# Kernel tuning notes

Measured on AMD Instinct MI355X. Metric: run time of the kernel, lower is better.

## Reference

```python
import jax, jax.numpy as jnp
import numpy as np

IN_F, OUT_F, RANK = 4096, 4096, 1024
B, S = 4, 2048


def soft_threshold24(w):
    """Soft-threshold 2:4 sparsification along the last dim.
    For each group of 4, the two smallest-magnitude entries are zeroed and the
    kept entries are shrunk by the threshold (2nd-smallest magnitude)."""
    g = w.reshape(-1, 4)
    m = jnp.abs(g)
    t = jnp.sort(m, axis=-1)[:, 1:2]  # largest pruned magnitude per group
    sp = jnp.sign(g) * jnp.maximum(m - t, 0.0)
    return sp.reshape(w.shape)


def fake_fp8_mm(a, b):
    """FP8-simulated GEMM: fp16 operands, fp32 accumulate/output (matches fake_fp8_mm)."""
    return jnp.matmul(a.astype(jnp.float16), b.astype(jnp.float16),
                      preferred_element_type=jnp.float32)


def setup_inputs() -> dict:
    key = jax.random.key(0)
    k1, k2, k3 = jax.random.split(key, 3)
    x = jax.random.normal(k1, (B, S, IN_F), dtype=jnp.float32)
    std_a = (2.0 / (IN_F + RANK)) ** 0.5   # xavier_normal for (in_features, rank)
    std_b = (2.0 / (OUT_F + RANK)) ** 0.5  # xavier_normal for (out_features, rank)
    weight_A = jax.random.normal(k2, (IN_F, RANK), dtype=jnp.float32) * std_a
    weight_B = jax.random.normal(k3, (OUT_F, RANK), dtype=jnp.float32) * std_b
    bias = jnp.zeros((OUT_F,), dtype=jnp.float32)
    scale_A = jnp.ones((), dtype=jnp.float32)  # sparse_init_scale buffer
    scale_B = jnp.ones((), dtype=jnp.float32)
    return {"x": x, "weight_A": weight_A, "weight_B": weight_B, "bias": bias,
            "scale_A": scale_A, "scale_B": scale_B}


def reference(x, weight_A, weight_B, bias, scale_A, scale_B):
    # sparse low-rank factors
    wa = soft_threshold24(weight_A) * scale_A  # (in, rank)
    wb = soft_threshold24(weight_B) * scale_B  # (out, rank)
    lead = x.shape[:-1]
    xf = x.reshape(-1, x.shape[-1])            # (T, in)
    x_proj = fake_fp8_mm(xf, wa)               # (T, rank) == x @ A_sparse
    out = fake_fp8_mm(x_proj, wb.T) + bias     # (T, out) == x_proj @ B_sparse^T + b
    return out.reshape(*lead, OUT_F)
```

## Files before the change

### kernel.cpp

```cpp
#include <hip/hip_runtime.h>

#define IN_FEAT 4096
#define OUT_FEAT 4096
#define RANK 1024
#define TOK 8192

typedef _Float16 f16x8 __attribute__((ext_vector_type(8)));
typedef _Float16 f16x4 __attribute__((ext_vector_type(4)));
typedef float f32x4 __attribute__((ext_vector_type(4)));

#define GLD_LDS16(g, l)                                                         \
  __builtin_amdgcn_global_load_lds(                                             \
      (__attribute__((address_space(1))) const void*)(g),                       \
      (__attribute__((address_space(3))) void*)(l), 16, 0, 0)


__device__ __forceinline__ void soft24(const float4 g, float s,
                                       float& r0, float& r1, float& r2, float& r3) {
  const float m0 = fabsf(g.x), m1 = fabsf(g.y), m2 = fabsf(g.z), m3 = fabsf(g.w);
  const float lo1 = fminf(m0, m1), hi1 = fmaxf(m0, m1);
  const float lo2 = fminf(m2, m3), hi2 = fmaxf(m2, m3);
  const float t = fminf(fmaxf(lo1, lo2), fminf(hi1, hi2));
  r0 = copysignf(fmaxf(m0 - t, 0.0f), g.x) * s;
  r1 = copysignf(fmaxf(m1 - t, 0.0f), g.y) * s;
  r2 = copysignf(fmaxf(m2 - t, 0.0f), g.z) * s;
  r3 = copysignf(fmaxf(m3 - t, 0.0f), g.w) * s;
}

__global__ __launch_bounds__(256) void sparsify_A_kernel(
    const float* __restrict__ wA, const float* __restrict__ scaleA,
    _Float16* __restrict__ waT) {
  const int idx = blockIdx.x * 256 + threadIdx.x;
  const int i = idx & (IN_FEAT - 1);
  const int jg = idx >> 12;
  const float4 g = *reinterpret_cast<const float4*>(wA + (size_t)i * RANK + jg * 4);
  const float s = scaleA[0];
  float r0, r1, r2, r3;
  soft24(g, s, r0, r1, r2, r3);
  const size_t base = (size_t)(jg * 4) * IN_FEAT + i;
  waT[base] = (_Float16)r0;
  waT[base + IN_FEAT] = (_Float16)r1;
  waT[base + 2 * IN_FEAT] = (_Float16)r2;
  waT[base + 3 * IN_FEAT] = (_Float16)r3;
}

__global__ __launch_bounds__(256) void sparsify_B_kernel(
    const float* __restrict__ wB, const float* __restrict__ scaleB,
    _Float16* __restrict__ wbs) {
  const int idx = blockIdx.x * 256 + threadIdx.x;
  const float4 g = *reinterpret_cast<const float4*>(wB + (size_t)idx * 4);
  const float s = scaleB[0];
  float r0, r1, r2, r3;
  soft24(g, s, r0, r1, r2, r3);
  f16x4 h;
  h[0] = (_Float16)r0; h[1] = (_Float16)r1; h[2] = (_Float16)r2; h[3] = (_Float16)r3;
  *reinterpret_cast<f16x4*>(wbs + (size_t)idx * 4) = h;
}

__global__ __launch_bounds__(256) void cast_x_kernel(
    const float* __restrict__ x, _Float16* __restrict__ x16) {
  const size_t i = ((size_t)blockIdx.x * 256 + threadIdx.x) * 8;
  const float4 f0 = *reinterpret_cast<const float4*>(x + i);
  const float4 f1 = *reinterpret_cast<const float4*>(x + i + 4);
  f16x8 h;
  h[0] = (_Float16)f0.x; h[1] = (_Float16)f0.y;
  h[2] = (_Float16)f0.z; h[3] = (_Float16)f0.w;
  h[4] = (_Float16)f1.x; h[5] = (_Float16)f1.y;
  h[6] = (_Float16)f1.z; h[7] = (_Float16)f1.w;
  *reinterpret_cast<f16x8*>(x16 + i) = h;
}

template <int N, int K, bool A_F32, bool OUT_F16>
__global__ __launch_bounds__(256, 4) void gemm128(
    const void* __restrict__ Av, const _Float16* __restrict__ Bh,
    void* __restrict__ Cv, const float* __restrict__ bias) {
  __shared__ __attribute__((aligned(128))) char lds[32768];
  char* ldsA = lds;
  char* ldsB = lds + 16384;

  const int tid = threadIdx.x;
  const int lane = tid & 63;
  const int w = tid >> 6;
  const int wrow = (w >> 1) * 64;
  const int wcol = (w & 1) * 64;

  constexpr int GX = N / 128;
  const int nwg = GX * (TOK / 128);
  const int l = blockIdx.y * GX + blockIdx.x;
  const int wg = (l & 7) * (nwg >> 3) + (l >> 3);
  const int brow = (wg / GX) * 128;
  const int bcol = (wg % GX) * 128;

  f32x4 acc[4][4] = {};

  for (int k0 = 0; k0 < K; k0 += 64) {
    __syncthreads();
#pragma unroll
    for (int it = 0; it < 4; ++it) {
      const int c = it * 256 + tid;
      const int row = c >> 3;
      const int u = c & 7;
      const _Float16* gsrc =
          Bh + (size_t)(bcol + row) * K + k0 + ((u ^ (row & 7)) << 3);
      GLD_LDS16(gsrc, ldsB + c * 16);
    }
    if constexpr (A_F32) {
      const float* Af = (const float*)Av;
#pragma unroll
      for (int it = 0; it < 4; ++it) {
        const int c = it * 256 + tid;
        const int row = c >> 3;
        const int u = c & 7;
        const float* gsrc = Af + (size_t)(brow + row) * K + k0 + (u << 3);
        const float4 f0 = *reinterpret_cast<const float4*>(gsrc);
        const float4 f1 = *reinterpret_cast<const float4*>(gsrc + 4);
        f16x8 h;
        h[0] = (_Float16)f0.x; h[1] = (_Float16)f0.y;
        h[2] = (_Float16)f0.z; h[3] = (_Float16)f0.w;
        h[4] = (_Float16)f1.x; h[5] = (_Float16)f1.y;
        h[6] = (_Float16)f1.z; h[7] = (_Float16)f1.w;
        *reinterpret_cast<f16x8*>(ldsA + row * 128 + ((u ^ (row & 7)) << 4)) = h;
      }
    } else {
      const _Float16* Ah = (const _Float16*)Av;
#pragma unroll
      for (int it = 0; it < 4; ++it) {
        const int c = it * 256 + tid;
        const int row = c >> 3;
        const int u = c & 7;
        const _Float16* gsrc =
            Ah + (size_t)(brow + row) * K + k0 + ((u ^ (row & 7)) << 3);
        GLD_LDS16(gsrc, ldsA + c * 16);
      }
    }
    __syncthreads();
#pragma unroll
    for (int kk = 0; kk < 2; ++kk) {
      f16x8 af[4], bf[4];
#pragma unroll
      for (int m = 0; m < 4; ++m) {
        const int row = wrow + m * 16 + (lane & 15);
        const int u = (kk * 4 + (lane >> 4)) ^ (row & 7);
        af[m] = *reinterpret_cast<const f16x8*>(ldsA + row * 128 + u * 16);
      }
#pragma unroll
      for (int n = 0; n < 4; ++n) {
        const int row = wcol + n * 16 + (lane & 15);
        const int u = (kk * 4 + (lane >> 4)) ^ (row & 7);
        bf[n] = *reinterpret_cast<const f16x8*>(ldsB + row * 128 + u * 16);
      }
#pragma unroll
      for (int m = 0; m < 4; ++m)
#pragma unroll
        for (int n = 0; n < 4; ++n)
          acc[m][n] =
              __builtin_amdgcn_mfma_f32_16x16x32_f16(af[m], bf[n], acc[m][n], 0, 0, 0);
    }
  }

  const int r4 = (lane >> 4) * 4;
  const int cl = lane & 15;
  if constexpr (OUT_F16) {
    _Float16* C = (_Float16*)Cv;
#pragma unroll
    for (int m = 0; m < 4; ++m)
#pragma unroll
      for (int n = 0; n < 4; ++n)
#pragma unroll
        for (int j = 0; j < 4; ++j) {
          const int rr = brow + wrow + m * 16 + r4 + j;
          const int cc = bcol + wcol + n * 16 + cl;
          C[(size_t)rr * N + cc] = (_Float16)acc[m][n][j];
        }
  } else {
    float* C = (float*)Cv;
#pragma unroll
    for (int n = 0; n < 4; ++n) {
      const int cc = bcol + wcol + n * 16 + cl;
      const float bv = bias[cc];
#pragma unroll
      for (int m = 0; m < 4; ++m)
#pragma unroll
        for (int j = 0; j < 4; ++j) {
          const int rr = brow + wrow + m * 16 + r4 + j;
          C[(size_t)rr * N + cc] = acc[m][n][j] + bv;
        }
    }
  }
}


extern "C" void kernel_launch(void* const* d_in, const int* in_sizes, int n_in,
                              void* d_out, int out_size, void* d_ws, size_t ws_size,
                              hipStream_t stream) {
  const float* x = (const float*)d_in[0];
  const float* wA = (const float*)d_in[1];
  const float* wB = (const float*)d_in[2];
  const float* bias = (const float*)d_in[3];
  const float* scaleA = (const float*)d_in[4];
  const float* scaleB = (const float*)d_in[5];
  float* out = (float*)d_out;

  char* ws = (char*)d_ws;
  _Float16* waT = (_Float16*)ws;
  _Float16* wbs = (_Float16*)(ws + (size_t)RANK * IN_FEAT * 2);
  _Float16* xp =
      (_Float16*)(ws + (size_t)RANK * IN_FEAT * 2 + (size_t)OUT_FEAT * RANK * 2);
  _Float16* x16 = (_Float16*)(ws + (size_t)RANK * IN_FEAT * 2 +
                              (size_t)OUT_FEAT * RANK * 2 + (size_t)TOK * RANK * 2);
  const size_t needed = (size_t)RANK * IN_FEAT * 2 + (size_t)OUT_FEAT * RANK * 2 +
                        (size_t)TOK * RANK * 2 + (size_t)TOK * IN_FEAT * 2;

  hipLaunchKernelGGL(sparsify_A_kernel, dim3((IN_FEAT * RANK / 4) / 256), dim3(256),
                     0, stream, wA, scaleA, waT);
  hipLaunchKernelGGL(sparsify_B_kernel, dim3((OUT_FEAT * RANK / 4) / 256), dim3(256),
                     0, stream, wB, scaleB, wbs);

  if (ws_size >= needed) {
    hipLaunchKernelGGL(cast_x_kernel, dim3((TOK * IN_FEAT / 8) / 256), dim3(256),
                       0, stream, x, x16);
    hipLaunchKernelGGL((gemm128<RANK, IN_FEAT, false, true>),
                       dim3(RANK / 128, TOK / 128), dim3(256), 0, stream,
                       (const void*)x16, waT, (void*)xp, nullptr);
  } else {
    hipLaunchKernelGGL((gemm128<RANK, IN_FEAT, true, true>),
                       dim3(RANK / 128, TOK / 128), dim3(256), 0, stream,
                       (const void*)x, waT, (void*)xp, nullptr);
  }

  hipLaunchKernelGGL((gemm128<OUT_FEAT, RANK, false, false>),
                     dim3(OUT_FEAT / 128, TOK / 128), dim3(256), 0, stream,
                     (const void*)xp, wbs, (void*)out, bias);
}
```

Baseline: 214.0 us.

## Replace second GEMM with 256x256-tile, 8-wave, double-buffered pipelined kernel

Adds a gemm256 kernel for the x_proj @ B^T stage. It uses 256x256 output tiles across 512 threads with 128KB of dynamic LDS, double-buffered across k-steps, and interleaves async global-to-LDS loads with MFMA quads under s_setprio and split barriers. The goal is to hide load latency and raise operand reuse per tile compared with the 128x128 single-buffered kernel. In exchange it uses more LDS and registers, so occupancy drops to 2 blocks, and the hand-written vmcnt waits must stay in step with the staging order.

Measured after the change: 206.2 us. -3.7%, faster.

```diff
diff --git a/kernel.cpp b/kernel.cpp
--- a/kernel.cpp
+++ b/kernel.cpp
@@ -189,6 +189,161 @@
   }
 }
 
+#define AOFF(s, h) (((s) * 2 + (h)) * 16384)
+#define BOFF(s, h) (65536 + ((s) * 2 + (h)) * 16384)
+
+#define MIDBAR()                                        \
+  __builtin_amdgcn_s_barrier();                         \
+  asm volatile("s_waitcnt lgkmcnt(0)" ::: "memory")
+#define ENDBAR() __builtin_amdgcn_s_barrier()
+
+#define QUAD(AF, BF, MO, NO)                                                   \
+  __builtin_amdgcn_s_setprio(1);                                               \
+  _Pragma("unroll") for (int ks = 0; ks < 2; ++ks)                             \
+  _Pragma("unroll") for (int i = 0; i < 4; ++i)                                \
+  _Pragma("unroll") for (int j = 0; j < 2; ++j)                                \
+      acc[(MO) + i][(NO) + j] = __builtin_amdgcn_mfma_f32_16x16x32_f16(        \
+          AF[i][ks], BF[j][ks], acc[(MO) + i][(NO) + j], 0, 0, 0);             \
+  __builtin_amdgcn_s_setprio(0);
+
+template <int M, int N, int K>
+__global__ __launch_bounds__(512, 2) void gemm256(
+    const _Float16* __restrict__ A, const _Float16* __restrict__ B,
+    float* __restrict__ C, const float* __restrict__ bias) {
+  extern __shared__ char lds[];
+
+  const int tid = threadIdx.x;
+  const int lane = tid & 63;
+  const int w = tid >> 6;
+  const int wr = w >> 2;
+  const int wc = w & 3;
+  const int l15 = lane & 15;
+  const int ubase = lane >> 4;
+
+  constexpr int GX = N / 256;
+  constexpr int NWG = GX * (M / 256);
+  const int l = blockIdx.y * GX + blockIdx.x;
+  const int wg = (l & 7) * (NWG >> 3) + (l >> 3);
+  const int brow = (wg / GX) * 256;
+  const int bcol = (wg % GX) * 256;
+
+  const _Float16* Abase = A + (size_t)brow * K;
+  const _Float16* Bbase = B + (size_t)bcol * K;
+
+  auto stage = [&](const _Float16* srcBase, int rowOff, int kof, int ldsOff) {
+#pragma unroll
+    for (int r = 0; r < 2; ++r) {
+      const int c = r * 512 + tid;
+      const int row = c >> 3;
+      const int u = c & 7;
+      const _Float16* g =
+          srcBase + (size_t)(rowOff + row) * K + kof + ((u ^ (row & 7)) << 3);
+      GLD_LDS16(g, lds + ldsOff + c * 16);
+    }
+  };
+
+  f32x4 acc[8][4] = {};
+  f16x8 af[4][2], bf01[2][2], bf23[2][2];
+
+#define LDA_GRP(SLOT, MBASE)                                                   \
+  _Pragma("unroll") for (int i = 0; i < 4; ++i)                                \
+  _Pragma("unroll") for (int ks = 0; ks < 2; ++ks) {                           \
+    const int row = ((MBASE) + i) * 16 + l15;                                  \
+    const int u = (ks * 4 + ubase) ^ (row & 7);                                \
+    af[i][ks] = *reinterpret_cast<const f16x8*>(                               \
+        lds + AOFF(SLOT, wr) + row * 128 + u * 16);                            \
+  }
+#define LDB_GRP(SLOT, NBASE, DST)                                              \
+  _Pragma("unroll") for (int j = 0; j < 2; ++j)                                \
+  _Pragma("unroll") for (int ks = 0; ks < 2; ++ks) {                           \
+    const int row = (wc & 1) * 64 + ((NBASE) + j) * 16 + l15;                  \
+    const int u = (ks * 4 + ubase) ^ (row & 7);                                \
+    DST[j][ks] = *reinterpret_cast<const f16x8*>(                              \
+        lds + BOFF(SLOT, wc >> 1) + row * 128 + u * 16);                       \
+  }
+
+  constexpr int NT = K / 64;
+
+  stage(Abase, 0, 0, AOFF(0, 0));
+  stage(Abase, 128, 0, AOFF(0, 1));
+  stage(Bbase, 0, 0, BOFF(0, 0));
+  stage(Bbase, 128, 0, BOFF(0, 1));
+  stage(Bbase, 0, 64, BOFF(1, 0));
+  stage(Bbase, 128, 64, BOFF(1, 1));
+  asm volatile("s_waitcnt vmcnt(4)" ::: "memory");
+  __builtin_amdgcn_s_barrier();
+
+  for (int tt = 0; tt < NT; tt += 2) {
+    const bool last = (tt + 2 >= NT);
+    const int kof1 = tt * 64 + 64;
+    const int kof2 = tt * 64 + 128;
+    const int kof3 = tt * 64 + 192;
+
+    LDA_GRP(0, 0);
+    LDB_GRP(0, 0, bf01);
+    stage(Abase, 0, kof1, AOFF(1, 0));
+    MIDBAR();
+    QUAD(af, bf01, 0, 0);
+    ENDBAR();
+    LDB_GRP(0, 2, bf23);
+    stage(Abase, 128, kof1, AOFF(1, 1));
+    MIDBAR();
+    QUAD(af, bf23, 0, 2);
+    ENDBAR();
+    LDA_GRP(0, 4);
+    if (!last) stage(Bbase, 0, kof2, BOFF(0, 0));
+    MIDBAR();
+    QUAD(af, bf01, 4, 0);
+    ENDBAR();
+    if (!last) {
+      stage(Bbase, 128, kof2, BOFF(0, 1));
+      asm volatile("s_waitcnt vmcnt(4)" ::: "memory");
+    } else {
+      asm volatile("s_waitcnt vmcnt(0)" ::: "memory");
+    }
+    MIDBAR();
+    QUAD(af, bf23, 4, 2);
+    ENDBAR();
+    LDA_GRP(1, 0);
+    LDB_GRP(1, 0, bf01);
+    if (!last) stage(Abase, 0, kof2, AOFF(0, 0));
+    MIDBAR();
+    QUAD(af, bf01, 0, 0);
+    ENDBAR();
+    LDB_GRP(1, 2, bf23);
+    if (!last) stage(Abase, 128, kof2, AOFF(0, 1));
+    MIDBAR();
+    QUAD(af, bf23, 0, 2);
+    ENDBAR();
+    LDA_GRP(1, 4);
+    if (!last) stage(Bbase, 0, kof3, BOFF(1, 0));
+    MIDBAR();
+    QUAD(af, bf01, 4, 0);
+    ENDBAR();
+    if (!last) {
+      stage(Bbase, 128, kof3, BOFF(1, 1));
+      asm volatile("s_waitcnt vmcnt(4)" ::: "memory");
+    }
+    MIDBAR();
+    QUAD(af, bf23, 4, 2);
+    ENDBAR();
+  }
+
+  const int r4 = (lane >> 4) * 4;
+#pragma unroll
+  for (int n = 0; n < 4; ++n) {
+    const int cc = bcol + wc * 64 + n * 16 + l15;
+    const float bv = bias[cc];
+#pragma unroll
+    for (int m = 0; m < 8; ++m)
+#pragma unroll
+      for (int j = 0; j < 4; ++j) {
+        const int rr = brow + wr * 128 + m * 16 + r4 + j;
+        C[(size_t)rr * N + cc] = acc[m][n][j] + bv;
+      }
+  }
+}
+
 
 extern "C" void kernel_launch(void* const* d_in, const int* in_sizes, int n_in,
                               void* d_out, int out_size, void* d_ws, size_t ws_size,
@@ -228,7 +383,10 @@
                        (const void*)x, waT, (void*)xp, nullptr);
   }
 
-  hipLaunchKernelGGL((gemm128<OUT_FEAT, RANK, false, false>),
-                     dim3(OUT_FEAT / 128, TOK / 128), dim3(256), 0, stream,
-                     (const void*)xp, wbs, (void*)out, bias);
-}
+  (void)hipFuncSetAttribute(
+      reinterpret_cast<const void*>(&gemm256<TOK, OUT_FEAT, RANK>),
+      hipFuncAttributeMaxDynamicSharedMemorySize, 131072);
+  hipLaunchKernelGGL((gemm256<TOK, OUT_FEAT, RANK>),
+                     dim3(OUT_FEAT / 256, TOK / 256), dim3(512), 131072, stream,
+                     xp, wbs, out, bias);
+}
```

## Add triple-buffered GEMM with direct register A loads and fused fp32 cast

Applied to the files above, without the earlier changes.

Introduces a new GEMM kernel that triple-buffers B tiles in LDS via async global-to-LDS loads, prefetching two stages ahead with one barrier per iteration. The A operand is loaded straight from global memory into registers, so only B goes through LDS. For the first GEMM this lets it read fp32 x and convert it in registers, removing the separate cast kernel and its fp16 intermediate buffer. It also swaps the MFMA operand order so results are written with vectorized stores. Risks are uncoalesced direct global A loads, higher register pressure (occupancy hint lowered to 2), and redundant A reads across workgroups.

Result: slower. 447.6 us (+109.2%).

```diff
diff --git a/kernel.cpp b/kernel.cpp
--- a/kernel.cpp
+++ b/kernel.cpp
@@ -57,19 +57,6 @@
   *reinterpret_cast<f16x4*>(wbs + (size_t)idx * 4) = h;
 }
 
-__global__ __launch_bounds__(256) void cast_x_kernel(
-    const float* __restrict__ x, _Float16* __restrict__ x16) {
-  const size_t i = ((size_t)blockIdx.x * 256 + threadIdx.x) * 8;
-  const float4 f0 = *reinterpret_cast<const float4*>(x + i);
-  const float4 f1 = *reinterpret_cast<const float4*>(x + i + 4);
-  f16x8 h;
-  h[0] = (_Float16)f0.x; h[1] = (_Float16)f0.y;
-  h[2] = (_Float16)f0.z; h[3] = (_Float16)f0.w;
-  h[4] = (_Float16)f1.x; h[5] = (_Float16)f1.y;
-  h[6] = (_Float16)f1.z; h[7] = (_Float16)f1.w;
-  *reinterpret_cast<f16x8*>(x16 + i) = h;
-}
-
 template <int N, int K, bool A_F32, bool OUT_F16>
 __global__ __launch_bounds__(256, 4) void gemm128(
     const void* __restrict__ Av, const _Float16* __restrict__ Bh,
@@ -189,6 +176,153 @@
   }
 }
 
+template <int M, int N, int K, bool A_F32, bool OUT_F16>
+__global__ __launch_bounds__(256, 2) void gemm_d(
+    const void* __restrict__ Av, const _Float16* __restrict__ Bh,
+    void* __restrict__ Cv, const float* __restrict__ bias) {
+  __shared__ __attribute__((aligned(128))) char lds[49152];
+
+  const int tid = threadIdx.x;
+  const int lane = tid & 63;
+  const int w = tid >> 6;
+  const int wr = w >> 1;
+  const int wc = w & 1;
+  const int l15 = lane & 15;
+  const int ubase = lane >> 4;
+
+  constexpr int GX = N / 128;
+  constexpr int NWG = GX * (M / 128);
+  const int l = blockIdx.y * GX + blockIdx.x;
+  const int wg = (l & 7) * (NWG >> 3) + (l >> 3);
+  const int brow = (wg / GX) * 128;
+  const int bcol = (wg % GX) * 128;
+
+  const _Float16* Ah = (const _Float16*)Av;
+  const float* Af = (const float*)Av;
+  const int arow = brow + wr * 64 + l15;
+  const int acol = ubase * 8;
+
+  f32x4 acc[4][4] = {};
+  f16x8 af[4][2], bf[4][2];
+  float4 areg[4][2][2];
+
+  auto stageB = [&](int kof, int slot) {
+#pragma unroll
+    for (int r = 0; r < 4; ++r) {
+      const int c = r * 256 + tid;
+      const int row = c >> 3, u = c & 7;
+      GLD_LDS16(Bh + (size_t)(bcol + row) * K + kof + ((u ^ (row & 7)) << 3),
+                lds + slot * 16384 + c * 16);
+    }
+  };
+
+  constexpr int NT = K / 64;
+
+  stageB(0, 0);
+  stageB(64, 1);
+  asm volatile("s_waitcnt vmcnt(4)" ::: "memory");
+  __builtin_amdgcn_s_barrier();
+
+  int slot = 0;
+  for (int t = 0; t < NT; ++t) {
+    __builtin_amdgcn_sched_barrier(0);
+    const int kc = t * 64 + acol;
+    if constexpr (A_F32) {
+#pragma unroll
+      for (int i = 0; i < 4; ++i)
+#pragma unroll
+        for (int ks = 0; ks < 2; ++ks) {
+          const float* p = Af + (size_t)(arow + i * 16) * K + kc + ks * 32;
+          areg[i][ks][0] = *reinterpret_cast<const float4*>(p);
+          areg[i][ks][1] = *reinterpret_cast<const float4*>(p + 4);
+        }
+    } else {
+#pragma unroll
+      for (int i = 0; i < 4; ++i)
+#pragma unroll
+        for (int ks = 0; ks < 2; ++ks)
+          af[i][ks] = *reinterpret_cast<const f16x8*>(
+              Ah + (size_t)(arow + i * 16) * K + kc + ks * 32);
+    }
+    if (t + 2 < NT) {
+      int s2 = slot + 2;
+      if (s2 >= 3) s2 -= 3;
+      stageB((t + 2) * 64, s2);
+    }
+#pragma unroll
+    for (int j = 0; j < 4; ++j)
+#pragma unroll
+      for (int ks = 0; ks < 2; ++ks) {
+        const int rb = wc * 64 + j * 16 + l15;
+        const int ub = (ks * 4 + ubase) ^ (rb & 7);
+        bf[j][ks] = *reinterpret_cast<const f16x8*>(lds + slot * 16384 +
+                                                    rb * 128 + ub * 16);
+      }
+    if constexpr (A_F32) {
+#pragma unroll
+      for (int i = 0; i < 4; ++i)
+#pragma unroll
+        for (int ks = 0; ks < 2; ++ks) {
+          f16x8 h;
+          h[0] = (_Float16)areg[i][ks][0].x; h[1] = (_Float16)areg[i][ks][0].y;
+          h[2] = (_Float16)areg[i][ks][0].z; h[3] = (_Float16)areg[i][ks][0].w;
+          h[4] = (_Float16)areg[i][ks][1].x; h[5] = (_Float16)areg[i][ks][1].y;
+          h[6] = (_Float16)areg[i][ks][1].z; h[7] = (_Float16)areg[i][ks][1].w;
+          af[i][ks] = h;
+        }
+    }
+    asm volatile("s_waitcnt lgkmcnt(0)" ::: "memory");
+    __builtin_amdgcn_sched_barrier(0);
+    __builtin_amdgcn_s_setprio(1);
+#pragma unroll
+    for (int ks = 0; ks < 2; ++ks)
+#pragma unroll
+      for (int i = 0; i < 4; ++i)
+#pragma unroll
+        for (int j = 0; j < 4; ++j)
+          acc[i][j] = __builtin_amdgcn_mfma_f32_16x16x32_f16(
+              bf[j][ks], af[i][ks], acc[i][j], 0, 0, 0);
+    __builtin_amdgcn_s_setprio(0);
+    if (t + 2 < NT) {
+      asm volatile("s_waitcnt vmcnt(4)" ::: "memory");
+    } else {
+      asm volatile("s_waitcnt vmcnt(0)" ::: "memory");
+    }
+    __builtin_amdgcn_s_barrier();
+    ++slot;
+    if (slot == 3) slot = 0;
+  }
+
+  const int r4 = (lane >> 4) * 4;
+  if constexpr (OUT_F16) {
+    _Float16* C = (_Float16*)Cv;
+#pragma unroll
+    for (int m = 0; m < 4; ++m)
+#pragma unroll
+      for (int n = 0; n < 4; ++n) {
+        const int rr = brow + wr * 64 + m * 16 + l15;
+        const int cc = bcol + wc * 64 + n * 16 + r4;
+        f16x4 h;
+#pragma unroll
+        for (int j = 0; j < 4; ++j) h[j] = (_Float16)acc[m][n][j];
+        *reinterpret_cast<f16x4*>(C + (size_t)rr * N + cc) = h;
+      }
+  } else {
+    float* C = (float*)Cv;
+#pragma unroll
+    for (int n = 0; n < 4; ++n) {
+      const int cc = bcol + wc * 64 + n * 16 + r4;
+      const f32x4 bv = *reinterpret_cast<const f32x4*>(bias + cc);
+#pragma unroll
+      for (int m = 0; m < 4; ++m) {
+        const int rr = brow + wr * 64 + m * 16 + l15;
+        f32x4 o = acc[m][n] + bv;
+        *reinterpret_cast<f32x4*>(C + (size_t)rr * N + cc) = o;
+      }
+    }
+  }
+}
+
 
 extern "C" void kernel_launch(void* const* d_in, const int* in_sizes, int n_in,
                               void* d_out, int out_size, void* d_ws, size_t ws_size,
@@ -206,10 +340,8 @@
   _Float16* wbs = (_Float16*)(ws + (size_t)RANK * IN_FEAT * 2);
   _Float16* xp =
       (_Float16*)(ws + (size_t)RANK * IN_FEAT * 2 + (size_t)OUT_FEAT * RANK * 2);
-  _Float16* x16 = (_Float16*)(ws + (size_t)RANK * IN_FEAT * 2 +
-                              (size_t)OUT_FEAT * RANK * 2 + (size_t)TOK * RANK * 2);
   const size_t needed = (size_t)RANK * IN_FEAT * 2 + (size_t)OUT_FEAT * RANK * 2 +
-                        (size_t)TOK * RANK * 2 + (size_t)TOK * IN_FEAT * 2;
+                        (size_t)TOK * RANK * 2;
 
   hipLaunchKernelGGL(sparsify_A_kernel, dim3((IN_FEAT * RANK / 4) / 256), dim3(256),
                      0, stream, wA, scaleA, waT);
@@ -217,18 +349,18 @@
                      0, stream, wB, scaleB, wbs);
 
   if (ws_size >= needed) {
-    hipLaunchKernelGGL(cast_x_kernel, dim3((TOK * IN_FEAT / 8) / 256), dim3(256),
-                       0, stream, x, x16);
-    hipLaunchKernelGGL((gemm128<RANK, IN_FEAT, false, true>),
+    hipLaunchKernelGGL((gemm_d<TOK, RANK, IN_FEAT, true, true>),
                        dim3(RANK / 128, TOK / 128), dim3(256), 0, stream,
-                       (const void*)x16, waT, (void*)xp, nullptr);
+                       (const void*)x, waT, (void*)xp, nullptr);
+    hipLaunchKernelGGL((gemm_d<TOK, OUT_FEAT, RANK, false, false>),
+                       dim3(OUT_FEAT / 128, TOK / 128), dim3(256), 0, stream,
+                       (const void*)xp, wbs, (void*)out, bias);
   } else {
     hipLaunchKernelGGL((gemm128<RANK, IN_FEAT, true, true>),
                        dim3(RANK / 128, TOK / 128), dim3(256), 0, stream,
                        (const void*)x, waT, (void*)xp, nullptr);
-  }
-
-  hipLaunchKernelGGL((gemm128<OUT_FEAT, RANK, false, false>),
-                     dim3(OUT_FEAT / 128, TOK / 128), dim3(256), 0, stream,
-                     (const void*)xp, wbs, (void*)out, bias);
-}
+    hipLaunchKernelGGL((gemm128<OUT_FEAT, RANK, false, false>),
+                       dim3(OUT_FEAT / 128, TOK / 128), dim3(256), 0, stream,
+                       (const void*)xp, wbs, (void*)out, bias);
+  }
+}
```
